# Performance work log

Hardware: AMD Instinct MI355X
Metric: run time of the kernel (lower is better)

The kernel has to match this reference:

```python
import jax, jax.numpy as jnp
import numpy as np
from jax.scipy.special import logsumexp

LOG_2PI = float(np.log(2.0 * np.pi))
ALPHA, BETA, GAMMA = 1.0, 1.0, 1.0


def gaussian_log_density(samples, mean, log_var):
    # -0.5 * ((x-mu)^2 * exp(-log_var) + log_var + log(2*pi)), elementwise
    tmp = samples - mean
    return -0.5 * (tmp * tmp * jnp.exp(-log_var) + log_var + LOG_2PI)


def log_importance_weight_matrix(batch_size, dataset_size):
    # Minibatch stratified sampling importance weights (rtqichen/beta-tcvae)
    N = dataset_size
    M = batch_size - 1
    strat_weight = (N - M) / (N * M)
    W_flat = jnp.full((batch_size * batch_size,), 1.0 / M, dtype=jnp.float32)
    idx_diag = np.arange(0, batch_size ** 2, M + 1)
    idx_off = np.arange(1, batch_size ** 2, M + 1)
    W_flat = W_flat.at[idx_diag].set(1.0 / N)
    W_flat = W_flat.at[idx_off].set(strat_weight)
    W = W_flat.reshape(batch_size, batch_size)
    W = W.at[M - 1, 0].set(strat_weight)
    return jnp.log(W)


def setup_inputs() -> dict:
    key = jax.random.key(0)
    ks = jax.random.split(key, 5)
    B, D, T = 2048, 32, 512
    return {
        "reconstruction": jax.random.normal(ks[0], (B, T), dtype=jnp.float32),
        "x": jax.random.normal(ks[1], (B, T), dtype=jnp.float32),
        "mu": jax.random.normal(ks[2], (B, D), dtype=jnp.float32),
        "log_var": jax.random.normal(ks[3], (B, D), dtype=jnp.float32) * 0.5,
        "z": jax.random.normal(ks[4], (B, D), dtype=jnp.float32),
        "dataset_size": 50000,
    }


def reference(reconstruction, x, mu, log_var, z, dataset_size):
    B = z.shape[0]
    # keras MAE: mean over last axis, then mean over batch == global mean |.|
    recon_loss = jnp.mean(jnp.abs(x - reconstruction))

    # log q(z|x): density of each sample under its own posterior, sum latent dims
    log_q_z_given_x = jnp.sum(gaussian_log_density(z, mu, log_var), axis=1)  # [B]

    # pairwise densities: sample i under posterior j -> [B, B, D]
    log_qz_prob = gaussian_log_density(z[:, None, :], mu[None, :, :], log_var[None, :, :])

    # log prior: N(0, e^1) per original code (log_var = ones_like(z))
    log_prior = jnp.sum(
        gaussian_log_density(z, jnp.zeros_like(z), jnp.ones_like(z)), axis=1
    )  # [B]

    # MSS branch
    logiw_mat = log_importance_weight_matrix(B, dataset_size)  # [B, B]
    # log q(z): logsumexp over posteriors of joint density (sum over latent dims)
    log_qz = logsumexp(logiw_mat + jnp.sum(log_qz_prob, axis=2), axis=1)  # [B]
    # log prod_d q(z_d): per-dim logsumexp over posteriors, then sum dims
    log_qz_product = jnp.sum(
        logsumexp(logiw_mat[:, :, None] + log_qz_prob, axis=1), axis=1
    )  # [B]

    mutual_info_loss = jnp.mean(log_q_z_given_x - log_qz)
    tc_loss = jnp.mean(log_qz - log_qz_product)
    dimension_wise_kl = jnp.mean(log_qz_product - log_prior)

    kl_loss = ALPHA * mutual_info_loss + BETA * tc_loss + GAMMA * dimension_wise_kl
    total_loss = recon_loss + kl_loss
    return (total_loss, recon_loss, kl_loss)
```

## Files before the change

kernel.cpp:

```cpp
#include <hip/hip_runtime.h>


#define B_SZ      2048
#define T_SZ      512
#define D_SZ      32
#define N_RECON4  (B_SZ * T_SZ / 4)
#define N_KL4     (B_SZ * D_SZ / 4)
#define NBLOCKS   256

__device__ __forceinline__ float kl_elem(float z, float m, float lv) {
    float t = z - m;
    return -0.5f * (t * t * __expf(-lv) + lv)
         + 0.5f * (z * z * 0.36787944117144233f + 1.0f);
}

__global__ __launch_bounds__(256) void tcvae_partial(
    const float* __restrict__ recon, const float* __restrict__ x,
    const float* __restrict__ mu, const float* __restrict__ lv,
    const float* __restrict__ z, float* __restrict__ partials)
{
    const int tid = blockIdx.x * blockDim.x + threadIdx.x;
    const int stride = gridDim.x * blockDim.x;

    float racc = 0.0f, kacc = 0.0f;

    const float4* x4 = (const float4*)x;
    const float4* r4 = (const float4*)recon;
    for (int i = tid; i < N_RECON4; i += stride) {
        float4 a = x4[i], b = r4[i];
        racc += fabsf(a.x - b.x) + fabsf(a.y - b.y)
              + fabsf(a.z - b.z) + fabsf(a.w - b.w);
    }

    const float4* z4 = (const float4*)z;
    const float4* m4 = (const float4*)mu;
    const float4* l4 = (const float4*)lv;
    for (int i = tid; i < N_KL4; i += stride) {
        float4 zz = z4[i], mm = m4[i], ll = l4[i];
        kacc += kl_elem(zz.x, mm.x, ll.x) + kl_elem(zz.y, mm.y, ll.y)
              + kl_elem(zz.z, mm.z, ll.z) + kl_elem(zz.w, mm.w, ll.w);
    }

    #pragma unroll
    for (int off = 32; off > 0; off >>= 1) {
        racc += __shfl_down(racc, off, 64);
        kacc += __shfl_down(kacc, off, 64);
    }

    __shared__ float sr[4], sk[4];
    const int lane = threadIdx.x & 63;
    const int wid  = threadIdx.x >> 6;
    if (lane == 0) { sr[wid] = racc; sk[wid] = kacc; }
    __syncthreads();
    if (threadIdx.x == 0) {
        partials[blockIdx.x]           = sr[0] + sr[1] + sr[2] + sr[3];
        partials[NBLOCKS + blockIdx.x] = sk[0] + sk[1] + sk[2] + sk[3];
    }
}

__global__ __launch_bounds__(256) void tcvae_final(
    const float* __restrict__ partials, float* __restrict__ out)
{
    float racc = 0.0f, kacc = 0.0f;
    for (int i = threadIdx.x; i < NBLOCKS; i += 256) {
        racc += partials[i];
        kacc += partials[NBLOCKS + i];
    }

    #pragma unroll
    for (int off = 32; off > 0; off >>= 1) {
        racc += __shfl_down(racc, off, 64);
        kacc += __shfl_down(kacc, off, 64);
    }

    __shared__ float sr[4], sk[4];
    const int lane = threadIdx.x & 63;
    const int wid  = threadIdx.x >> 6;
    if (lane == 0) { sr[wid] = racc; sk[wid] = kacc; }
    __syncthreads();
    if (threadIdx.x == 0) {
        float r = (sr[0] + sr[1] + sr[2] + sr[3]) * (1.0f / (float)(B_SZ * T_SZ));
        float k = (sk[0] + sk[1] + sk[2] + sk[3]) * (1.0f / (float)B_SZ);
        out[0] = r + k;
        out[1] = r;
        out[2] = k;
    }
}

extern "C" void kernel_launch(void* const* d_in, const int* in_sizes, int n_in,
                              void* d_out, int out_size, void* d_ws, size_t ws_size,
                              hipStream_t stream) {
    const float* recon = (const float*)d_in[0];
    const float* x     = (const float*)d_in[1];
    const float* mu    = (const float*)d_in[2];
    const float* lv    = (const float*)d_in[3];
    const float* z     = (const float*)d_in[4];

    float* partials = (float*)d_ws;
    float* out      = (float*)d_out;

    tcvae_partial<<<NBLOCKS, 256, 0, stream>>>(recon, x, mu, lv, z, partials);
    tcvae_final<<<1, 256, 0, stream>>>(partials, out);
}
```

Before: 69.77 us.

## Fuse partial and final reductions into one cooperative kernel with grid sync

Replaces the two-kernel reduction (per-block partials, then a single-block final sum) with one kernel launched cooperatively. After writing its partials, each block does a threadfence and a grid-wide sync, and block 0 then reduces the partials and writes the outputs. The recon loop now has a compile-time trip count and is fully unrolled, and the KL loop becomes a single guarded load. This removes one kernel launch and the gap between kernels, at the cost of a cooperative launch and a grid barrier, which on HIP can carry their own overhead.

```diff
diff --git a/kernel.cpp b/kernel.cpp
--- a/kernel.cpp
+++ b/kernel.cpp
@@ -1,4 +1,7 @@
 #include <hip/hip_runtime.h>
+#include <hip/hip_cooperative_groups.h>
+
+namespace cg = cooperative_groups;
 
 
 #define B_SZ      2048
@@ -7,6 +10,8 @@
 #define N_RECON4  (B_SZ * T_SZ / 4)
 #define N_KL4     (B_SZ * D_SZ / 4)
 #define NBLOCKS   256
+#define NTHREADS  256
+#define STRIDE    (NBLOCKS * NTHREADS)
 
 __device__ __forceinline__ float kl_elem(float z, float m, float lv) {
     float t = z - m;
@@ -14,31 +19,32 @@
          + 0.5f * (z * z * 0.36787944117144233f + 1.0f);
 }
 
-__global__ __launch_bounds__(256) void tcvae_partial(
+__global__ __launch_bounds__(NTHREADS) void tcvae_fused(
     const float* __restrict__ recon, const float* __restrict__ x,
     const float* __restrict__ mu, const float* __restrict__ lv,
-    const float* __restrict__ z, float* __restrict__ partials)
+    const float* __restrict__ z, float* __restrict__ partials,
+    float* __restrict__ out)
 {
-    const int tid = blockIdx.x * blockDim.x + threadIdx.x;
-    const int stride = gridDim.x * blockDim.x;
+    const int tid = blockIdx.x * NTHREADS + threadIdx.x;
 
     float racc = 0.0f, kacc = 0.0f;
 
     const float4* x4 = (const float4*)x;
     const float4* r4 = (const float4*)recon;
-    for (int i = tid; i < N_RECON4; i += stride) {
+    #pragma unroll
+    for (int k = 0; k < N_RECON4 / STRIDE; ++k) {
+        const int i = tid + k * STRIDE;
         float4 a = x4[i], b = r4[i];
         racc += fabsf(a.x - b.x) + fabsf(a.y - b.y)
               + fabsf(a.z - b.z) + fabsf(a.w - b.w);
     }
 
-    const float4* z4 = (const float4*)z;
-    const float4* m4 = (const float4*)mu;
-    const float4* l4 = (const float4*)lv;
-    for (int i = tid; i < N_KL4; i += stride) {
-        float4 zz = z4[i], mm = m4[i], ll = l4[i];
-        kacc += kl_elem(zz.x, mm.x, ll.x) + kl_elem(zz.y, mm.y, ll.y)
-              + kl_elem(zz.z, mm.z, ll.z) + kl_elem(zz.w, mm.w, ll.w);
+    if (tid < N_KL4) {
+        float4 zz = ((const float4*)z)[tid];
+        float4 mm = ((const float4*)mu)[tid];
+        float4 ll = ((const float4*)lv)[tid];
+        kacc = kl_elem(zz.x, mm.x, ll.x) + kl_elem(zz.y, mm.y, ll.y)
+             + kl_elem(zz.z, mm.z, ll.z) + kl_elem(zz.w, mm.w, ll.w);
     }
 
     #pragma unroll
@@ -56,34 +62,30 @@
         partials[blockIdx.x]           = sr[0] + sr[1] + sr[2] + sr[3];
         partials[NBLOCKS + blockIdx.x] = sk[0] + sk[1] + sk[2] + sk[3];
     }
-}
+    __threadfence();
 
-__global__ __launch_bounds__(256) void tcvae_final(
-    const float* __restrict__ partials, float* __restrict__ out)
-{
-    float racc = 0.0f, kacc = 0.0f;
-    for (int i = threadIdx.x; i < NBLOCKS; i += 256) {
-        racc += partials[i];
-        kacc += partials[NBLOCKS + i];
-    }
+    cg::this_grid().sync();
 
-    #pragma unroll
-    for (int off = 32; off > 0; off >>= 1) {
-        racc += __shfl_down(racc, off, 64);
-        kacc += __shfl_down(kacc, off, 64);
-    }
-
-    __shared__ float sr[4], sk[4];
-    const int lane = threadIdx.x & 63;
-    const int wid  = threadIdx.x >> 6;
-    if (lane == 0) { sr[wid] = racc; sk[wid] = kacc; }
-    __syncthreads();
-    if (threadIdx.x == 0) {
-        float r = (sr[0] + sr[1] + sr[2] + sr[3]) * (1.0f / (float)(B_SZ * T_SZ));
-        float k = (sk[0] + sk[1] + sk[2] + sk[3]) * (1.0f / (float)B_SZ);
-        out[0] = r + k;
-        out[1] = r;
-        out[2] = k;
+    if (blockIdx.x == 0) {
+        float r2 = 0.0f, k2 = 0.0f;
+        for (int i = threadIdx.x; i < NBLOCKS; i += NTHREADS) {
+            r2 += partials[i];
+            k2 += partials[NBLOCKS + i];
+        }
+        #pragma unroll
+        for (int off = 32; off > 0; off >>= 1) {
+            r2 += __shfl_down(r2, off, 64);
+            k2 += __shfl_down(k2, off, 64);
+        }
+        if (lane == 0) { sr[wid] = r2; sk[wid] = k2; }
+        __syncthreads();
+        if (threadIdx.x == 0) {
+            float r = (sr[0] + sr[1] + sr[2] + sr[3]) * (1.0f / (float)(B_SZ * T_SZ));
+            float k = (sk[0] + sk[1] + sk[2] + sk[3]) * (1.0f / (float)B_SZ);
+            out[0] = r + k;
+            out[1] = r;
+            out[2] = k;
+        }
     }
 }
 
@@ -99,6 +101,9 @@
     float* partials = (float*)d_ws;
     float* out      = (float*)d_out;
 
-    tcvae_partial<<<NBLOCKS, 256, 0, stream>>>(recon, x, mu, lv, z, partials);
-    tcvae_final<<<1, 256, 0, stream>>>(partials, out);
+    void* args[] = { (void*)&recon, (void*)&x, (void*)&mu, (void*)&lv,
+                     (void*)&z, (void*)&partials, (void*)&out };
+    hipLaunchCooperativeKernel((const void*)tcvae_fused,
+                               dim3(NBLOCKS), dim3(NTHREADS),
+                               args, 0, stream);
 }
```

After: 119.9 us. 71.9% more time.
